# Optimization experiments

Hardware: AMD Instinct MI355X
Metric: run time of the kernel (lower is better)

The kernel has to match this reference:

```python
import jax, jax.numpy as jnp
import numpy as np

NUM_HEADS = 12
LN_EPS = 1e-12


def setup_inputs() -> dict:
    key = jax.random.key(0)
    ks = jax.random.split(key, 18)
    B, S, H, I, P, KW = 8, 128, 768, 3072, 50, 100
    s = 0.02
    inp = {
        'hidden_state': jax.random.normal(ks[0], (B, S, H), jnp.float32),
        'positive_keywords': jax.random.normal(ks[1], (P, H), jnp.float32),
        'negative_keywords': jax.random.normal(ks[2], (P, H), jnp.float32),
        'attention_mask': jnp.zeros((B, 1, 1, S), jnp.float32),
        # Bilinear weights: out = (x @ W) * keyword
        'Wq': jax.random.normal(ks[3], (H, H), jnp.float32) * s,
        'Wk': jax.random.normal(ks[4], (H, H), jnp.float32) * s,
        'Wv': jax.random.normal(ks[5], (H, H), jnp.float32) * s,
        'Wo': jax.random.normal(ks[6], (H, H), jnp.float32) * s,
        'bo': jnp.zeros((H,), jnp.float32),
        # mlp: Linear(kwcount, 1)
        'Wmlp': jax.random.normal(ks[7], (KW,), jnp.float32) * s,
        'bmlp': jnp.zeros((), jnp.float32),
        # Bottleneck FFN
        'Wdown': jax.random.normal(ks[8], (H, I), jnp.float32) * s,
        'bdown': jnp.zeros((I,), jnp.float32),
        'Wup': jax.random.normal(ks[9], (I, H), jnp.float32) * s,
        'bup': jnp.zeros((H,), jnp.float32),
        'gamma': jnp.ones((H,), jnp.float32),
        'beta': jnp.zeros((H,), jnp.float32),
    }
    return inp


def reference(hidden_state, positive_keywords, negative_keywords, attention_mask,
              Wq, Wk, Wv, Wo, bo, Wmlp, bmlp, Wdown, bdown, Wup, bup, gamma, beta):
    B, S, H = hidden_state.shape
    nh = NUM_HEADS
    hd = H // nh
    # interleave pos/neg keywords -> pool [KW, H] (diff == 0, no padding)
    pool = jnp.stack((positive_keywords, negative_keywords), axis=1).reshape(-1, H)

    # shared sequence projections (keyword modulates elementwise afterwards)
    PQ = hidden_state @ Wq  # [B,S,H]
    PK = hidden_state @ Wk
    PV = hidden_state @ Wv
    scale = 1.0 / jnp.sqrt(jnp.float32(hd))

    def per_kw(kw):  # kw: [H]
        def heads(P):
            return (P * kw).reshape(B, S, nh, hd).transpose(0, 2, 1, 3)  # [B,nh,S,hd]
        Q, K, V = heads(PQ), heads(PK), heads(PV)
        scores = jnp.einsum('bhqd,bhkd->bhqk', Q, K) * scale + attention_mask
        # NOTE: softmax over dim=-2 (query axis), faithful to the original
        w = jax.nn.softmax(scores, axis=-2)
        ctx = jnp.einsum('bhqk,bhkd->bhqd', w, V)
        ctx = ctx.transpose(0, 2, 1, 3).reshape(B, S, H)
        return ctx @ Wo + bo  # [B,S,H]

    stacked = jax.vmap(per_kw)(pool)  # [KW,B,S,H]
    # mlp Linear(KW,1) over the stacked keyword axis
    fused = jnp.einsum('kbsh,k->bsh', stacked, Wmlp) + bmlp  # [B,S,H]

    # Bottleneck FFN + residual LayerNorm (dropout = identity in eval)
    down = jax.nn.gelu(fused @ Wdown + bdown, approximate=False)
    up = down @ Wup + bup
    x = up + fused
    mu = jnp.mean(x, axis=-1, keepdims=True)
    var = jnp.var(x, axis=-1, keepdims=True)
    return gamma * (x - mu) / jnp.sqrt(var + LN_EPS) + beta
```

## Files before the change

kernel.cpp:

```cpp
#include <hip/hip_runtime.h>
#include <hip/hip_bf16.h>
#include <math.h>

#define B_ 8
#define S_ 128
#define H_ 768
#define NH_ 12
#define HD_ 64
#define M_ 1024
#define KW_ 100
#define I_ 3072
#define QKVN 2304
#define NCHUNK 10
#define KWPER 10
#define LOG2E 1.4426950408889634f

typedef __attribute__((ext_vector_type(8))) short short8;
typedef __attribute__((ext_vector_type(8))) unsigned short ushort8;
typedef __attribute__((ext_vector_type(4))) float f32x4;

static __device__ __forceinline__ unsigned short f2b(float f) {
  union { float f; unsigned int u; } v; v.f = f;
  return (unsigned short)((v.u + 0x7fffu + ((v.u >> 16) & 1u)) >> 16);
}
static __device__ __forceinline__ float b2f(unsigned short b) {
  union { unsigned int u; float f; } v; v.u = ((unsigned int)b) << 16;
  return v.f;
}

__global__ void k_prep(const float* __restrict__ hidden,
                       const float* __restrict__ Wq, const float* __restrict__ Wk,
                       const float* __restrict__ Wv, const float* __restrict__ Wo,
                       const float* __restrict__ Wdown, const float* __restrict__ Wup,
                       const float* __restrict__ posk, const float* __restrict__ negk,
                       const float* __restrict__ Wmlp, const float* __restrict__ bmlp,
                       const float* __restrict__ bo,
                       unsigned short* __restrict__ hb, unsigned short* __restrict__ qkvT,
                       unsigned short* __restrict__ WoT, unsigned short* __restrict__ WdownT,
                       unsigned short* __restrict__ WupT,
                       float* __restrict__ kw2s, float* __restrict__ kwm, float* __restrict__ c0) {
  __shared__ float tile[32][33];
  int z = blockIdx.z;
  int t = threadIdx.x;
  if (z == 6) {
    int n = blockIdx.y * 96 + blockIdx.x;
    if (n < 768) {
      int i = (n * 256 + t) * 4;
      float4 v = *(const float4*)&hidden[i];
      uint2 o;
      o.x = (unsigned)f2b(v.x) | ((unsigned)f2b(v.y) << 16);
      o.y = (unsigned)f2b(v.z) | ((unsigned)f2b(v.w) << 16);
      *(uint2*)&hb[i] = o;
    } else if (n < 1068) {
      int idx = (n - 768) * 256 + t;
      if (idx < KW_ * H_) {
        int j = idx / H_, d = idx - j * H_;
        float v = (j & 1) ? negk[(j >> 1) * H_ + d] : posk[(j >> 1) * H_ + d];
        kw2s[idx] = v * v * 0.125f * LOG2E;
        kwm[idx] = v * Wmlp[j];
      }
    } else if (n == 1068) {
      __shared__ float red[256];
      red[t] = (t < KW_) ? Wmlp[t] : 0.f;
      __syncthreads();
      for (int s = 128; s > 0; s >>= 1) { if (t < s) red[t] += red[t + s]; __syncthreads(); }
      float sWm = red[0];
      for (int c = t; c < H_; c += 256) c0[c] = sWm * bo[c] + bmlp[0];
    }
    return;
  }
  const float* src; unsigned short* dst; int R, C, r0, c0t;
  if (z < 4) {
    if (blockIdx.x >= 24) return;
    const float* srcs[4] = {Wq, Wk, Wv, Wo};
    src = srcs[z];
    dst = (z < 3) ? qkvT + (size_t)z * 768 * 768 : WoT;
    R = 768; C = 768; c0t = blockIdx.x * 32; r0 = blockIdx.y * 32;
  } else if (z == 4) {
    src = Wdown; dst = WdownT; R = 768; C = 3072;
    c0t = blockIdx.x * 32; r0 = blockIdx.y * 32;
  } else {
    src = Wup; dst = WupT; R = 3072; C = 768;
    c0t = blockIdx.y * 32; r0 = blockIdx.x * 32;
  }
  int tx = t & 31, ty = t >> 5;
#pragma unroll
  for (int i = 0; i < 4; i++)
    tile[ty + i * 8][tx] = src[(size_t)(r0 + ty + i * 8) * C + c0t + tx];
  __syncthreads();
#pragma unroll
  for (int i = 0; i < 4; i++)
    dst[(size_t)(c0t + ty + i * 8) * R + r0 + tx] = f2b(tile[tx][ty + i * 8]);
}

template <int EPI>
__launch_bounds__(256)
__global__ void k_gemm_bt(const unsigned short* __restrict__ A, const unsigned short* __restrict__ BT,
                          int M, int N, int K,
                          float* __restrict__ outF, unsigned short* __restrict__ outB,
                          const float* __restrict__ bias, const float* __restrict__ res) {
  __shared__ unsigned short Asm[128][56];
  __shared__ unsigned short Bsm[128][56];
  int tid = threadIdx.x;
  int lane = tid & 63, wid = tid >> 6;
  int g = lane >> 4, c16 = lane & 15;
  int wr = wid >> 1, wc = wid & 1;
  int m0 = blockIdx.y * 128, n0 = blockIdx.x * 128;
  f32x4 acc[4][4] = {};
  int r = tid >> 1, half = (tid & 1) * 16;
  const unsigned short* Ap = A + (size_t)(m0 + r) * K + half;
  const unsigned short* Bp = BT + (size_t)(n0 + r) * K + half;
  for (int kt = 0; kt < K; kt += 32) {
    __syncthreads();
    ushort8 a0 = *(const ushort8*)(Ap + kt);
    ushort8 a1 = *(const ushort8*)(Ap + kt + 8);
    ushort8 b0 = *(const ushort8*)(Bp + kt);
    ushort8 b1 = *(const ushort8*)(Bp + kt + 8);
    *(ushort8*)&Asm[r][half] = a0;  *(ushort8*)&Asm[r][half + 8] = a1;
    *(ushort8*)&Bsm[r][half] = b0;  *(ushort8*)&Bsm[r][half + 8] = b1;
    __syncthreads();
    short8 af[4], bf[4];
#pragma unroll
    for (int mi = 0; mi < 4; mi++) af[mi] = *(const short8*)&Asm[wr * 64 + mi * 16 + c16][g * 8];
#pragma unroll
    for (int ni = 0; ni < 4; ni++) bf[ni] = *(const short8*)&Bsm[wc * 64 + ni * 16 + c16][g * 8];
#pragma unroll
    for (int mi = 0; mi < 4; mi++)
#pragma unroll
      for (int ni = 0; ni < 4; ni++)
        acc[mi][ni] = __builtin_amdgcn_mfma_f32_16x16x32_bf16(af[mi], bf[ni], acc[mi][ni], 0, 0, 0);
  }
#pragma unroll
  for (int mi = 0; mi < 4; mi++)
#pragma unroll
    for (int ni = 0; ni < 4; ni++)
#pragma unroll
      for (int rr = 0; rr < 4; rr++) {
        int row = m0 + wr * 64 + mi * 16 + g * 4 + rr;
        int col = n0 + wc * 64 + ni * 16 + c16;
        float v = acc[mi][ni][rr];
        if (EPI == 0) {
          outB[(size_t)row * N + col] = f2b(v);
        } else if (EPI == 2) {
          float t = v + bias[col];
          float gl = 0.5f * t * (1.f + erff(t * 0.70710678118f));
          outB[(size_t)row * N + col] = f2b(gl);
        }
      }
}

__launch_bounds__(256)
__global__ void k_gemm_sk(const unsigned short* __restrict__ A, const unsigned short* __restrict__ BT,
                          int M, int N, int K, int ksl, float* __restrict__ pOut) {
  __shared__ unsigned short Asm[128][56];
  __shared__ unsigned short Bsm[128][56];
  int tid = threadIdx.x;
  int lane = tid & 63, wid = tid >> 6;
  int g = lane >> 4, c16 = lane & 15;
  int wr = wid >> 1, wc = wid & 1;
  int m0 = blockIdx.y * 128, n0 = blockIdx.x * 128;
  int kstart = blockIdx.z * ksl;
  f32x4 acc[4][4] = {};
  int r = tid >> 1, half = (tid & 1) * 16;
  const unsigned short* Ap = A + (size_t)(m0 + r) * K + half + kstart;
  const unsigned short* Bp = BT + (size_t)(n0 + r) * K + half + kstart;
  for (int kt = 0; kt < ksl; kt += 32) {
    __syncthreads();
    ushort8 a0 = *(const ushort8*)(Ap + kt);
    ushort8 a1 = *(const ushort8*)(Ap + kt + 8);
    ushort8 b0 = *(const ushort8*)(Bp + kt);
    ushort8 b1 = *(const ushort8*)(Bp + kt + 8);
    *(ushort8*)&Asm[r][half] = a0;  *(ushort8*)&Asm[r][half + 8] = a1;
    *(ushort8*)&Bsm[r][half] = b0;  *(ushort8*)&Bsm[r][half + 8] = b1;
    __syncthreads();
    short8 af[4], bf[4];
#pragma unroll
    for (int mi = 0; mi < 4; mi++) af[mi] = *(const short8*)&Asm[wr * 64 + mi * 16 + c16][g * 8];
#pragma unroll
    for (int ni = 0; ni < 4; ni++) bf[ni] = *(const short8*)&Bsm[wc * 64 + ni * 16 + c16][g * 8];
#pragma unroll
    for (int mi = 0; mi < 4; mi++)
#pragma unroll
      for (int ni = 0; ni < 4; ni++)
        acc[mi][ni] = __builtin_amdgcn_mfma_f32_16x16x32_bf16(af[mi], bf[ni], acc[mi][ni], 0, 0, 0);
  }
  float* dst = pOut + (size_t)blockIdx.z * M * N;
#pragma unroll
  for (int mi = 0; mi < 4; mi++)
#pragma unroll
    for (int ni = 0; ni < 4; ni++)
#pragma unroll
      for (int rr = 0; rr < 4; rr++) {
        int row = m0 + wr * 64 + mi * 16 + g * 4 + rr;
        int col = n0 + wc * 64 + ni * 16 + c16;
        dst[(size_t)row * N + col] = acc[mi][ni][rr];
      }
}

template <int SPLITS, int EPI>
__global__ void k_red(const float* __restrict__ p, const float* __restrict__ bias,
                      float* __restrict__ outF, unsigned short* __restrict__ outB, int N) {
  int i = (blockIdx.x * 256 + threadIdx.x) * 4;
  const size_t MN = (size_t)M_ * N;
  float4 s = *(const float4*)&p[i];
#pragma unroll
  for (int c = 1; c < SPLITS; c++) {
    float4 v = *(const float4*)&p[c * MN + i];
    s.x += v.x; s.y += v.y; s.z += v.z; s.w += v.w;
  }
  if (EPI == 1) {
    int col = i % N;
    s.x += bias[col]; s.y += bias[col + 1]; s.z += bias[col + 2]; s.w += bias[col + 3];
    *(float4*)&outF[i] = s;
  }
  uint2 o;
  o.x = (unsigned)f2b(s.x) | ((unsigned)f2b(s.y) << 16);
  o.y = (unsigned)f2b(s.z) | ((unsigned)f2b(s.w) << 16);
  *(uint2*)&outB[i] = o;
}


static __device__ __forceinline__ int swzA(int r, int c) {
  return (((r << 7) + (c << 1)) ^ ((r & 7) << 4)) >> 1;
}
static __device__ __forceinline__ int swzW(int r, int c) {
  return (((r << 8) + (c << 1)) ^ (((r >> 1) & 7) << 4)) >> 1;
}

__launch_bounds__(512, 8)
__global__ void k_attn(const unsigned short* __restrict__ PQKV,
                       const float* __restrict__ kw2s, const float* __restrict__ kwm,
                       float* __restrict__ partial) {
  __shared__ unsigned short WLAS[128 * 128];
  __shared__ unsigned short PVT[64][136];
  __shared__ float kw2L[KWPER * 64];
  __shared__ unsigned short kwmL[KWPER * 64];
  int tid = threadIdx.x;
  int lane = tid & 63, wid = tid >> 6;
  int g = lane >> 4, c16 = lane & 15;
  int chunk = blockIdx.x, h = blockIdx.y, b = blockIdx.z;
  const size_t rowbase = (size_t)b * 128 * QKVN;
  int kq = tid >> 2, quarter = tid & 3;
  int kcol = wid * 16 + c16;
  ushort8 q0, q1;
  {
    const unsigned short* srcv = PQKV + rowbase + (size_t)kq * QKVN + 2 * H_ + h * HD_ + quarter * 16;
    ushort8 w0 = *(const ushort8*)srcv;
    ushort8 w1 = *(const ushort8*)(srcv + 8);
#pragma unroll
    for (int j = 0; j < 8; j++) PVT[quarter * 16 + j][kq] = w0[j];
#pragma unroll
    for (int j = 0; j < 8; j++) PVT[quarter * 16 + 8 + j][kq] = w1[j];
    const unsigned short* srcq = PQKV + rowbase + (size_t)kq * QKVN + h * HD_ + quarter * 16;
    q0 = *(const ushort8*)srcq;
    q1 = *(const ushort8*)(srcq + 8);
    for (int i = tid; i < KWPER * 64; i += 512) {
      int ki = i >> 6, d = i & 63;
      size_t gi = (size_t)(chunk * KWPER + ki) * H_ + h * HD_ + d;
      kw2L[i] = kw2s[gi];
      kwmL[i] = f2b(kwm[gi]);
    }
  }
  const unsigned short* bkp = PQKV + rowbase + (size_t)kcol * QKVN + H_ + h * HD_;
  __syncthreads();
  float accO[4][4] = {};
  for (int ki = 0; ki < KWPER; ki++) {
    ushort8 bk0 = *(const ushort8*)(bkp + g * 8);
    ushort8 bk1 = *(const ushort8*)(bkp + 32 + g * 8);
    {
      const float* kp = &kw2L[ki * 64 + quarter * 16];
      unsigned int o[8];
#pragma unroll
      for (int p = 0; p < 4; p++) {
        float2 cc = *(const float2*)&kp[2 * p];
        float lo = b2f(q0[2 * p]) * cc.x;
        float hi = b2f(q0[2 * p + 1]) * cc.y;
        asm("v_cvt_pk_bf16_f32 %0, %1, %2" : "=v"(o[p]) : "v"(lo), "v"(hi));
      }
#pragma unroll
      for (int p = 0; p < 4; p++) {
        float2 cc = *(const float2*)&kp[8 + 2 * p];
        float lo = b2f(q1[2 * p]) * cc.x;
        float hi = b2f(q1[2 * p + 1]) * cc.y;
        asm("v_cvt_pk_bf16_f32 %0, %1, %2" : "=v"(o[4 + p]) : "v"(lo), "v"(hi));
      }
      *(uint4*)&WLAS[swzA(kq, quarter * 16)] = *(const uint4*)&o[0];
      *(uint4*)&WLAS[swzA(kq, quarter * 16 + 8)] = *(const uint4*)&o[4];
    }
    __syncthreads();
    f32x4 sc[8];
    __builtin_amdgcn_s_setprio(1);
#pragma unroll
    for (int mi = 0; mi < 8; mi++) {
      short8 aq0 = *(const short8*)&WLAS[swzA(mi * 16 + c16, g * 8)];
      short8 aq1 = *(const short8*)&WLAS[swzA(mi * 16 + c16, 32 + g * 8)];
      f32x4 z = {0.f, 0.f, 0.f, 0.f};
      z = __builtin_amdgcn_mfma_f32_16x16x32_bf16(aq0, *(const short8*)&bk0, z, 0, 0, 0);
      z = __builtin_amdgcn_mfma_f32_16x16x32_bf16(aq1, *(const short8*)&bk1, z, 0, 0, 0);
      sc[mi] = z;
    }
    __builtin_amdgcn_s_setprio(0);
    float sm = 0.f;
#pragma unroll
    for (int mi = 0; mi < 8; mi++)
#pragma unroll
      for (int rr = 0; rr < 4; rr++) { float e = __builtin_amdgcn_exp2f(sc[mi][rr]); sc[mi][rr] = e; sm += e; }
    sm += __shfl_xor(sm, 16);
    sm += __shfl_xor(sm, 32);
    float rinv = 1.0f / sm;
    __syncthreads();
    unsigned baseoff = ((unsigned)(g * 4) << 8) + ((unsigned)(kcol & ~1) << 1);
    baseoff ^= (unsigned)(g * 32);
#pragma unroll
    for (int mi = 0; mi < 8; mi++) {
      float a0 = sc[mi][0] * rinv, a1 = sc[mi][1] * rinv;
      float a2 = sc[mi][2] * rinv, a3 = sc[mi][3] * rinv;
      unsigned pk0, pk1;
      asm("v_cvt_pk_bf16_f32 %0, %1, %2" : "=v"(pk0) : "v"(a0), "v"(a1));
      asm("v_cvt_pk_bf16_f32 %0, %1, %2" : "=v"(pk1) : "v"(a2), "v"(a3));
      unsigned px0 = __shfl_xor(pk0, 1);
      unsigned px1 = __shfl_xor(pk1, 1);
      if (!(lane & 1)) {
        unsigned w0 = (pk0 & 0xffffu) | (px0 << 16);
        unsigned w1 = (pk0 >> 16) | (px0 & 0xffff0000u);
        unsigned w2 = (pk1 & 0xffffu) | (px1 << 16);
        unsigned w3 = (pk1 >> 16) | (px1 & 0xffff0000u);
        unsigned off1 = baseoff + (unsigned)mi * 4096u;
        unsigned off2 = (off1 + 512u) ^ 16u;
        *(unsigned*)((char*)WLAS + off1) = w0;
        *(unsigned*)((char*)WLAS + off1 + 256) = w1;
        *(unsigned*)((char*)WLAS + off2) = w2;
        *(unsigned*)((char*)WLAS + off2 + 256) = w3;
      }
    }
    __syncthreads();
    short8 wf[4];
#pragma unroll
    for (int kc = 0; kc < 4; kc++) wf[kc] = *(const short8*)&WLAS[swzW(wid * 16 + c16, kc * 32 + g * 8)];
    __builtin_amdgcn_s_setprio(1);
    f32x4 zz[4];
#pragma unroll
    for (int ni = 0; ni < 4; ni++) {
      f32x4 z = {0.f, 0.f, 0.f, 0.f};
#pragma unroll
      for (int kc = 0; kc < 4; kc++) {
        short8 vf = *(const short8*)&PVT[ni * 16 + c16][kc * 32 + g * 8];
        z = __builtin_amdgcn_mfma_f32_16x16x32_bf16(wf[kc], vf, z, 0, 0, 0);
      }
      zz[ni] = z;
    }
    __builtin_amdgcn_s_setprio(0);
#pragma unroll
    for (int ni = 0; ni < 4; ni++) {
      float km = b2f(kwmL[ki * 64 + ni * 16 + c16]);
#pragma unroll
      for (int rr = 0; rr < 4; rr++) accO[ni][rr] += zz[ni][rr] * km;
    }
    __syncthreads();
  }
  float* dst = partial + (size_t)chunk * M_ * H_;
#pragma unroll
  for (int ni = 0; ni < 4; ni++)
#pragma unroll
    for (int rr = 0; rr < 4; rr++) {
      int q = wid * 16 + g * 4 + rr;
      dst[(size_t)(b * 128 + q) * H_ + h * HD_ + ni * 16 + c16] = accO[ni][rr];
    }
}

__global__ void k_reduce(const float* __restrict__ partial, unsigned short* __restrict__ ctxsum) {
  int i = (blockIdx.x * 256 + threadIdx.x) * 4;
  float4 s = *(const float4*)&partial[i];
#pragma unroll
  for (int c = 1; c < NCHUNK; c++) {
    float4 v = *(const float4*)&partial[(size_t)c * M_ * H_ + i];
    s.x += v.x; s.y += v.y; s.z += v.z; s.w += v.w;
  }
  uint2 o;
  o.x = (unsigned)f2b(s.x) | ((unsigned)f2b(s.y) << 16);
  o.y = (unsigned)f2b(s.z) | ((unsigned)f2b(s.w) << 16);
  *(uint2*)&ctxsum[i] = o;
}

__launch_bounds__(256)
__global__ void k_ln2(const float* __restrict__ pUp, const float* __restrict__ bup,
                      const float* __restrict__ fusedF,
                      const float* __restrict__ gamma, const float* __restrict__ beta,
                      float* __restrict__ out) {
  __shared__ float red[8];
  int row = blockIdx.x, t = threadIdx.x;
  int lane = t & 63, wid = t >> 6;
  const size_t MN = (size_t)M_ * H_;
  const size_t rb = (size_t)row * H_;
  float v[3];
#pragma unroll
  for (int j = 0; j < 3; j++) {
    int c = t + j * 256;
    float x = pUp[rb + c] + pUp[MN + rb + c] + pUp[2 * MN + rb + c] + pUp[3 * MN + rb + c];
    v[j] = x + bup[c] + fusedF[rb + c];
  }
  float s = v[0] + v[1] + v[2];
#pragma unroll
  for (int off = 1; off < 64; off <<= 1) s += __shfl_xor(s, off);
  if (lane == 0) red[wid] = s;
  __syncthreads();
  float mu = (red[0] + red[1] + red[2] + red[3]) * (1.f / 768.f);
  float q = 0.f;
#pragma unroll
  for (int j = 0; j < 3; j++) { float d = v[j] - mu; q += d * d; }
#pragma unroll
  for (int off = 1; off < 64; off <<= 1) q += __shfl_xor(q, off);
  if (lane == 0) red[4 + wid] = q;
  __syncthreads();
  float var = (red[4] + red[5] + red[6] + red[7]) * (1.f / 768.f);
  float rstd = rsqrtf(var + 1e-12f);
#pragma unroll
  for (int j = 0; j < 3; j++) {
    int c = t + j * 256;
    out[rb + c] = gamma[c] * ((v[j] - mu) * rstd) + beta[c];
  }
}


extern "C" void kernel_launch(void* const* d_in, const int* in_sizes, int n_in,
                              void* d_out, int out_size, void* d_ws, size_t ws_size,
                              hipStream_t stream) {
  const float* hidden = (const float*)d_in[0];
  const float* posk   = (const float*)d_in[1];
  const float* negk   = (const float*)d_in[2];
  const float* Wq     = (const float*)d_in[4];
  const float* Wk     = (const float*)d_in[5];
  const float* Wv     = (const float*)d_in[6];
  const float* Wo     = (const float*)d_in[7];
  const float* bo     = (const float*)d_in[8];
  const float* Wmlp   = (const float*)d_in[9];
  const float* bmlp   = (const float*)d_in[10];
  const float* Wdown  = (const float*)d_in[11];
  const float* bdown  = (const float*)d_in[12];
  const float* Wup    = (const float*)d_in[13];
  const float* bup    = (const float*)d_in[14];
  const float* gamma  = (const float*)d_in[15];
  const float* beta   = (const float*)d_in[16];

  char* ws = (char*)d_ws;
  size_t off = 0;
  auto alloc = [&](size_t bytes) -> void* {
    void* p = ws + off;
    off += (bytes + 255) & ~(size_t)255;
    return p;
  };
  unsigned short* hb     = (unsigned short*)alloc((size_t)M_ * H_ * 2);
  unsigned short* qkvT   = (unsigned short*)alloc((size_t)QKVN * H_ * 2);
  unsigned short* WoT    = (unsigned short*)alloc((size_t)H_ * H_ * 2);
  unsigned short* WdownT = (unsigned short*)alloc((size_t)I_ * H_ * 2);
  unsigned short* WupT   = (unsigned short*)alloc((size_t)H_ * I_ * 2);
  unsigned short* PQKV   = (unsigned short*)alloc((size_t)M_ * QKVN * 2);
  float* kw2s    = (float*)alloc((size_t)KW_ * H_ * 4);
  float* kwm     = (float*)alloc((size_t)KW_ * H_ * 4);
  float* c0      = (float*)alloc((size_t)H_ * 4);
  float* partial = (float*)alloc((size_t)NCHUNK * M_ * H_ * 4);
  unsigned short* ctxsum = (unsigned short*)alloc((size_t)M_ * H_ * 2);
  float* fusedF  = (float*)alloc((size_t)M_ * H_ * 4);
  unsigned short* fusedB = (unsigned short*)alloc((size_t)M_ * H_ * 2);
  unsigned short* downB  = (unsigned short*)alloc((size_t)M_ * I_ * 2);

  k_prep<<<dim3(96, 24, 7), 256, 0, stream>>>(hidden, Wq, Wk, Wv, Wo, Wdown, Wup,
                                              posk, negk, Wmlp, bmlp, bo,
                                              hb, qkvT, WoT, WdownT, WupT, kw2s, kwm, c0);
  k_gemm_sk<<<dim3(18, 8, 2), 256, 0, stream>>>(hb, qkvT, M_, QKVN, H_, 384, partial);
  k_red<2, 0><<<2304, 256, 0, stream>>>(partial, nullptr, nullptr, PQKV, QKVN);
  k_attn<<<dim3(NCHUNK, NH_, B_), 512, 0, stream>>>(PQKV, kw2s, kwm, partial);
  k_reduce<<<768, 256, 0, stream>>>(partial, ctxsum);
  k_gemm_sk<<<dim3(6, 8, 2), 256, 0, stream>>>(ctxsum, WoT, M_, H_, H_, 384, partial);
  k_red<2, 1><<<768, 256, 0, stream>>>(partial, c0, fusedF, fusedB, H_);
  k_gemm_bt<2><<<dim3(24, 8), 256, 0, stream>>>(fusedB, WdownT, M_, I_, H_, nullptr, downB, bdown, nullptr);
  k_gemm_sk<<<dim3(6, 8, 4), 256, 0, stream>>>(downB, WupT, M_, H_, I_, 768, partial);
  k_ln2<<<M_, 256, 0, stream>>>(partial, bup, fusedF, gamma, beta, (float*)d_out);
}
```

Measured before the change: 210.8 us.

## Restructure attention kernel to keep K and V fragments in registers per wave

The attention kernel now loads K and V tiles into registers once before the keyword loop. Each wave computes scores for its own 16 query rows against all keys and writes normalized weights to a private per-wave LDS buffer, which removes the shared-tile writes and two of the block barriers per keyword. The column-wise softmax sums are reduced across waves through a small SUMS/RINV buffer, which still costs two barriers per iteration. The trade is much higher register pressure (launch bounds dropped from 8 to 2), and the exponentials are rounded to bf16 before normalization, which adds some numerical error.

```diff
diff --git a/kernel.cpp b/kernel.cpp
--- a/kernel.cpp
+++ b/kernel.cpp
@@ -223,27 +223,30 @@
 static __device__ __forceinline__ int swzA(int r, int c) {
   return (((r << 7) + (c << 1)) ^ ((r & 7) << 4)) >> 1;
 }
-static __device__ __forceinline__ int swzW(int r, int c) {
-  return (((r << 8) + (c << 1)) ^ (((r >> 1) & 7) << 4)) >> 1;
-}
-
-__launch_bounds__(512, 8)
+
+__launch_bounds__(512, 2)
 __global__ void k_attn(const unsigned short* __restrict__ PQKV,
                        const float* __restrict__ kw2s, const float* __restrict__ kwm,
                        float* __restrict__ partial) {
-  __shared__ unsigned short WLAS[128 * 128];
+  __shared__ unsigned short Ks[128 * 64];
   __shared__ unsigned short PVT[64][136];
+  __shared__ unsigned short WL[8][16 * 128];
+  __shared__ float SUMS[8][128];
+  __shared__ float RINV[128];
   __shared__ float kw2L[KWPER * 64];
-  __shared__ unsigned short kwmL[KWPER * 64];
+  __shared__ float kwmL[KWPER * 64];
   int tid = threadIdx.x;
   int lane = tid & 63, wid = tid >> 6;
   int g = lane >> 4, c16 = lane & 15;
   int chunk = blockIdx.x, h = blockIdx.y, b = blockIdx.z;
   const size_t rowbase = (size_t)b * 128 * QKVN;
   int kq = tid >> 2, quarter = tid & 3;
-  int kcol = wid * 16 + c16;
-  ushort8 q0, q1;
   {
+    const unsigned short* srck = PQKV + rowbase + (size_t)kq * QKVN + H_ + h * HD_ + quarter * 16;
+    ushort8 v0 = *(const ushort8*)srck;
+    ushort8 v1 = *(const ushort8*)(srck + 8);
+    *(ushort8*)&Ks[swzA(kq, quarter * 16)] = v0;
+    *(ushort8*)&Ks[swzA(kq, quarter * 16 + 8)] = v1;
     const unsigned short* srcv = PQKV + rowbase + (size_t)kq * QKVN + 2 * H_ + h * HD_ + quarter * 16;
     ushort8 w0 = *(const ushort8*)srcv;
     ushort8 w1 = *(const ushort8*)(srcv + 8);
@@ -251,120 +254,138 @@
     for (int j = 0; j < 8; j++) PVT[quarter * 16 + j][kq] = w0[j];
 #pragma unroll
     for (int j = 0; j < 8; j++) PVT[quarter * 16 + 8 + j][kq] = w1[j];
-    const unsigned short* srcq = PQKV + rowbase + (size_t)kq * QKVN + h * HD_ + quarter * 16;
-    q0 = *(const ushort8*)srcq;
-    q1 = *(const ushort8*)(srcq + 8);
     for (int i = tid; i < KWPER * 64; i += 512) {
       int ki = i >> 6, d = i & 63;
       size_t gi = (size_t)(chunk * KWPER + ki) * H_ + h * HD_ + d;
       kw2L[i] = kw2s[gi];
-      kwmL[i] = f2b(kwm[gi]);
-    }
-  }
-  const unsigned short* bkp = PQKV + rowbase + (size_t)kcol * QKVN + H_ + h * HD_;
+      kwmL[i] = kwm[gi];
+    }
+  }
+  const unsigned short* qp = PQKV + rowbase + (size_t)(wid * 16 + c16) * QKVN + h * HD_;
+  ushort8 qf0 = *(const ushort8*)(qp + g * 8);
+  ushort8 qf1 = *(const ushort8*)(qp + 32 + g * 8);
   __syncthreads();
+  short8 kf[8][2];
+#pragma unroll
+  for (int t = 0; t < 8; t++)
+#pragma unroll
+    for (int s = 0; s < 2; s++)
+      kf[t][s] = *(const short8*)&Ks[swzA(t * 16 + c16, s * 32 + g * 8)];
+  short8 vf[4][4];
+#pragma unroll
+  for (int dt = 0; dt < 4; dt++)
+#pragma unroll
+    for (int s = 0; s < 4; s++)
+      vf[dt][s] = *(const short8*)&PVT[dt * 16 + c16][s * 32 + g * 8];
+  char* wbuf = (char*)&WL[wid][0];
   float accO[4][4] = {};
   for (int ki = 0; ki < KWPER; ki++) {
-    ushort8 bk0 = *(const ushort8*)(bkp + g * 8);
-    ushort8 bk1 = *(const ushort8*)(bkp + 32 + g * 8);
+    const float* kp = &kw2L[ki * 64];
+    short8 aA0, aA1;
     {
-      const float* kp = &kw2L[ki * 64 + quarter * 16];
-      unsigned int o[8];
-#pragma unroll
-      for (int p = 0; p < 4; p++) {
-        float2 cc = *(const float2*)&kp[2 * p];
-        float lo = b2f(q0[2 * p]) * cc.x;
-        float hi = b2f(q0[2 * p + 1]) * cc.y;
-        asm("v_cvt_pk_bf16_f32 %0, %1, %2" : "=v"(o[p]) : "v"(lo), "v"(hi));
+      float4 ka = *(const float4*)&kp[g * 8];
+      float4 kb = *(const float4*)&kp[g * 8 + 4];
+      float4 kc = *(const float4*)&kp[32 + g * 8];
+      float4 kd = *(const float4*)&kp[32 + g * 8 + 4];
+      union { unsigned u[4]; short8 v; } p0, p1;
+      asm("v_cvt_pk_bf16_f32 %0, %1, %2" : "=v"(p0.u[0]) : "v"(b2f(qf0[0]) * ka.x), "v"(b2f(qf0[1]) * ka.y));
+      asm("v_cvt_pk_bf16_f32 %0, %1, %2" : "=v"(p0.u[1]) : "v"(b2f(qf0[2]) * ka.z), "v"(b2f(qf0[3]) * ka.w));
+      asm("v_cvt_pk_bf16_f32 %0, %1, %2" : "=v"(p0.u[2]) : "v"(b2f(qf0[4]) * kb.x), "v"(b2f(qf0[5]) * kb.y));
+      asm("v_cvt_pk_bf16_f32 %0, %1, %2" : "=v"(p0.u[3]) : "v"(b2f(qf0[6]) * kb.z), "v"(b2f(qf0[7]) * kb.w));
+      asm("v_cvt_pk_bf16_f32 %0, %1, %2" : "=v"(p1.u[0]) : "v"(b2f(qf1[0]) * kc.x), "v"(b2f(qf1[1]) * kc.y));
+      asm("v_cvt_pk_bf16_f32 %0, %1, %2" : "=v"(p1.u[1]) : "v"(b2f(qf1[2]) * kc.z), "v"(b2f(qf1[3]) * kc.w));
+      asm("v_cvt_pk_bf16_f32 %0, %1, %2" : "=v"(p1.u[2]) : "v"(b2f(qf1[4]) * kd.x), "v"(b2f(qf1[5]) * kd.y));
+      asm("v_cvt_pk_bf16_f32 %0, %1, %2" : "=v"(p1.u[3]) : "v"(b2f(qf1[6]) * kd.z), "v"(b2f(qf1[7]) * kd.w));
+      aA0 = p0.v; aA1 = p1.v;
+    }
+    unsigned e[8][2];
+    float s8v[8];
+    __builtin_amdgcn_s_setprio(1);
+#pragma unroll
+    for (int t = 0; t < 8; t++) {
+      f32x4 z = {0.f, 0.f, 0.f, 0.f};
+      z = __builtin_amdgcn_mfma_f32_16x16x32_bf16(aA0, kf[t][0], z, 0, 0, 0);
+      z = __builtin_amdgcn_mfma_f32_16x16x32_bf16(aA1, kf[t][1], z, 0, 0, 0);
+      float e0 = __builtin_amdgcn_exp2f(z[0]);
+      float e1 = __builtin_amdgcn_exp2f(z[1]);
+      float e2 = __builtin_amdgcn_exp2f(z[2]);
+      float e3 = __builtin_amdgcn_exp2f(z[3]);
+      s8v[t] = (e0 + e1) + (e2 + e3);
+      asm("v_cvt_pk_bf16_f32 %0, %1, %2" : "=v"(e[t][0]) : "v"(e0), "v"(e1));
+      asm("v_cvt_pk_bf16_f32 %0, %1, %2" : "=v"(e[t][1]) : "v"(e2), "v"(e3));
+    }
+    __builtin_amdgcn_s_setprio(0);
+#pragma unroll
+    for (int t = 0; t < 8; t++) {
+      s8v[t] += __shfl_xor(s8v[t], 16);
+      s8v[t] += __shfl_xor(s8v[t], 32);
+    }
+    if (g == 0) {
+#pragma unroll
+      for (int t = 0; t < 8; t++) SUMS[wid][c16 + 16 * t] = s8v[t];
+    }
+    __syncthreads();
+    if (tid < 128) {
+      float tot = 0.f;
+#pragma unroll
+      for (int w = 0; w < 8; w++) tot += SUMS[w][tid];
+      RINV[tid] = 1.0f / tot;
+    }
+    __syncthreads();
+    {
+      int cb2 = c16 * 2;
+      int qb = g * 4;
+      int xb = (g & 1) * 4;
+#pragma unroll
+      for (int t = 0; t < 8; t++) {
+        float ri = RINV[c16 + 16 * t];
+        float w0 = b2f((unsigned short)(e[t][0] & 0xffffu)) * ri;
+        float w1 = b2f((unsigned short)(e[t][0] >> 16)) * ri;
+        float w2 = b2f((unsigned short)(e[t][1] & 0xffffu)) * ri;
+        float w3 = b2f((unsigned short)(e[t][1] >> 16)) * ri;
+        unsigned p01, p23;
+        asm("v_cvt_pk_bf16_f32 %0, %1, %2" : "=v"(p01) : "v"(w0), "v"(w1));
+        asm("v_cvt_pk_bf16_f32 %0, %1, %2" : "=v"(p23) : "v"(w2), "v"(w3));
+        int tb = t * 32 + cb2;
+        int a0 = ((qb + 0) * 256 + tb) ^ ((xb + 0) << 4);
+        int a1 = ((qb + 1) * 256 + tb) ^ ((xb + 1) << 4);
+        int a2 = ((qb + 2) * 256 + tb) ^ ((xb + 2) << 4);
+        int a3 = ((qb + 3) * 256 + tb) ^ ((xb + 3) << 4);
+        *(unsigned short*)(wbuf + a0) = (unsigned short)(p01 & 0xffffu);
+        *(unsigned short*)(wbuf + a1) = (unsigned short)(p01 >> 16);
+        *(unsigned short*)(wbuf + a2) = (unsigned short)(p23 & 0xffffu);
+        *(unsigned short*)(wbuf + a3) = (unsigned short)(p23 >> 16);
       }
-#pragma unroll
-      for (int p = 0; p < 4; p++) {
-        float2 cc = *(const float2*)&kp[8 + 2 * p];
-        float lo = b2f(q1[2 * p]) * cc.x;
-        float hi = b2f(q1[2 * p + 1]) * cc.y;
-        asm("v_cvt_pk_bf16_f32 %0, %1, %2" : "=v"(o[4 + p]) : "v"(lo), "v"(hi));
-      }
-      *(uint4*)&WLAS[swzA(kq, quarter * 16)] = *(const uint4*)&o[0];
-      *(uint4*)&WLAS[swzA(kq, quarter * 16 + 8)] = *(const uint4*)&o[4];
-    }
-    __syncthreads();
-    f32x4 sc[8];
-    __builtin_amdgcn_s_setprio(1);
-#pragma unroll
-    for (int mi = 0; mi < 8; mi++) {
-      short8 aq0 = *(const short8*)&WLAS[swzA(mi * 16 + c16, g * 8)];
-      short8 aq1 = *(const short8*)&WLAS[swzA(mi * 16 + c16, 32 + g * 8)];
-      f32x4 z = {0.f, 0.f, 0.f, 0.f};
-      z = __builtin_amdgcn_mfma_f32_16x16x32_bf16(aq0, *(const short8*)&bk0, z, 0, 0, 0);
-      z = __builtin_amdgcn_mfma_f32_16x16x32_bf16(aq1, *(const short8*)&bk1, z, 0, 0, 0);
-      sc[mi] = z;
-    }
-    __builtin_amdgcn_s_setprio(0);
-    float sm = 0.f;
-#pragma unroll
-    for (int mi = 0; mi < 8; mi++)
-#pragma unroll
-      for (int rr = 0; rr < 4; rr++) { float e = __builtin_amdgcn_exp2f(sc[mi][rr]); sc[mi][rr] = e; sm += e; }
-    sm += __shfl_xor(sm, 16);
-    sm += __shfl_xor(sm, 32);
-    float rinv = 1.0f / sm;
-    __syncthreads();
-    unsigned baseoff = ((unsigned)(g * 4) << 8) + ((unsigned)(kcol & ~1) << 1);
-    baseoff ^= (unsigned)(g * 32);
-#pragma unroll
-    for (int mi = 0; mi < 8; mi++) {
-      float a0 = sc[mi][0] * rinv, a1 = sc[mi][1] * rinv;
-      float a2 = sc[mi][2] * rinv, a3 = sc[mi][3] * rinv;
-      unsigned pk0, pk1;
-      asm("v_cvt_pk_bf16_f32 %0, %1, %2" : "=v"(pk0) : "v"(a0), "v"(a1));
-      asm("v_cvt_pk_bf16_f32 %0, %1, %2" : "=v"(pk1) : "v"(a2), "v"(a3));
-      unsigned px0 = __shfl_xor(pk0, 1);
-      unsigned px1 = __shfl_xor(pk1, 1);
-      if (!(lane & 1)) {
-        unsigned w0 = (pk0 & 0xffffu) | (px0 << 16);
-        unsigned w1 = (pk0 >> 16) | (px0 & 0xffff0000u);
-        unsigned w2 = (pk1 & 0xffffu) | (px1 << 16);
-        unsigned w3 = (pk1 >> 16) | (px1 & 0xffff0000u);
-        unsigned off1 = baseoff + (unsigned)mi * 4096u;
-        unsigned off2 = (off1 + 512u) ^ 16u;
-        *(unsigned*)((char*)WLAS + off1) = w0;
-        *(unsigned*)((char*)WLAS + off1 + 256) = w1;
-        *(unsigned*)((char*)WLAS + off2) = w2;
-        *(unsigned*)((char*)WLAS + off2 + 256) = w3;
-      }
-    }
-    __syncthreads();
+    }
     short8 wf[4];
 #pragma unroll
-    for (int kc = 0; kc < 4; kc++) wf[kc] = *(const short8*)&WLAS[swzW(wid * 16 + c16, kc * 32 + g * 8)];
+    for (int s = 0; s < 4; s++)
+      wf[s] = *(const short8*)(wbuf + ((c16 * 256 + s * 64 + g * 16) ^ ((c16 & 7) << 4)));
     __builtin_amdgcn_s_setprio(1);
     f32x4 zz[4];
 #pragma unroll
-    for (int ni = 0; ni < 4; ni++) {
+    for (int dt = 0; dt < 4; dt++) {
       f32x4 z = {0.f, 0.f, 0.f, 0.f};
 #pragma unroll
-      for (int kc = 0; kc < 4; kc++) {
-        short8 vf = *(const short8*)&PVT[ni * 16 + c16][kc * 32 + g * 8];
-        z = __builtin_amdgcn_mfma_f32_16x16x32_bf16(wf[kc], vf, z, 0, 0, 0);
-      }
-      zz[ni] = z;
+      for (int s = 0; s < 4; s++)
+        z = __builtin_amdgcn_mfma_f32_16x16x32_bf16(wf[s], vf[dt][s], z, 0, 0, 0);
+      zz[dt] = z;
     }
     __builtin_amdgcn_s_setprio(0);
 #pragma unroll
-    for (int ni = 0; ni < 4; ni++) {
-      float km = b2f(kwmL[ki * 64 + ni * 16 + c16]);
-#pragma unroll
-      for (int rr = 0; rr < 4; rr++) accO[ni][rr] += zz[ni][rr] * km;
-    }
-    __syncthreads();
+    for (int dt = 0; dt < 4; dt++) {
+      float km = kwmL[ki * 64 + dt * 16 + c16];
+#pragma unroll
+      for (int rr = 0; rr < 4; rr++) accO[dt][rr] += zz[dt][rr] * km;
+    }
   }
   float* dst = partial + (size_t)chunk * M_ * H_;
 #pragma unroll
-  for (int ni = 0; ni < 4; ni++)
+  for (int dt = 0; dt < 4; dt++)
 #pragma unroll
     for (int rr = 0; rr < 4; rr++) {
       int q = wid * 16 + g * 4 + rr;
-      dst[(size_t)(b * 128 + q) * H_ + h * HD_ + ni * 16 + c16] = accO[ni][rr];
+      dst[(size_t)(b * 128 + q) * H_ + h * HD_ + dt * 16 + c16] = accO[dt][rr];
     }
 }
 
```

Result: no change. 207.6 us (-1.5%).
